# Optimization experiments

Hardware: AMD Instinct MI355X
Metric: run time of the kernel (lower is better)

Reference implementation:

```python
import jax, jax.numpy as jnp
import numpy as np

M_MARGIN = 0.25
GAMMA = 256.0
NEG_INF = jnp.float32(-1e30)


def setup_inputs() -> dict:
    key = jax.random.key(0)
    k1, k2 = jax.random.split(key)
    feature = jax.random.normal(k1, (8192, 128), dtype=jnp.float32)
    label = jax.random.randint(k2, (8192,), 0, 64, dtype=jnp.int64)
    return {"feature": feature, "label": label}


def reference(feature, label):
    # F.normalize: L2-normalize rows (eps=1e-12)
    norm = jnp.maximum(jnp.linalg.norm(feature, axis=1, keepdims=True), 1e-12)
    f = feature / norm
    sim = f @ f.T  # [N, N]
    N = sim.shape[0]

    same = label[:, None] == label[None, :]
    triu = jnp.triu(jnp.ones((N, N), dtype=bool), k=1)
    pos_mask = same & triu
    neg_mask = (~same) & triu

    sim_d = jax.lax.stop_gradient(sim)  # .detach() in original
    ap = jnp.maximum(-sim_d + 1.0 + M_MARGIN, 0.0)
    an = jnp.maximum(sim_d + M_MARGIN, 0.0)
    delta_p = 1.0 - M_MARGIN
    delta_n = M_MARGIN

    logit_p = -ap * (sim - delta_p) * GAMMA
    logit_n = an * (sim - delta_n) * GAMMA

    # boolean-gather + logsumexp == masked logsumexp (fixed shapes, jit-friendly)
    lse_p = jax.nn.logsumexp(jnp.where(pos_mask, logit_p, NEG_INF))
    lse_n = jax.nn.logsumexp(jnp.where(neg_mask, logit_n, NEG_INF))

    return jax.nn.softplus(lse_n + lse_p)
```

## Files before the change

### kernel.cpp

```cpp
#include <hip/hip_runtime.h>
#include <hip/hip_bf16.h>
#include <math.h>

#define NROW 8192
#define DIM  128
#define BT   128
#define NT   (NROW / BT)
#define NBLK ((NT * (NT + 1)) / 2)
#define NT4  (NBLK * 8)
#define NRED   32
#define PERRED (NT4 / NRED)

typedef __bf16 bf16x8 __attribute__((ext_vector_type(8)));
typedef float  f32x4  __attribute__((ext_vector_type(4)));

#define G2     369.3299304675746f
#define QPOS   (0.9375f * G2)
#define QNEG   (-0.0625f * G2)
#define NEGBIG (-3.0e38f)
#define MSENT  (-4000.0f)

__global__ __launch_bounds__(256)
void prep_kernel(const float* __restrict__ f, __hip_bfloat16* __restrict__ fhi) {
    int row  = blockIdx.x * 4 + (threadIdx.x >> 6);
    int lane = threadIdx.x & 63;
    float2 v = ((const float2*)(f + (size_t)row * DIM))[lane];
    float ss = v.x * v.x + v.y * v.y;
    #pragma unroll
    for (int off = 32; off; off >>= 1) ss += __shfl_xor(ss, off, 64);
    float inv = 1.0f / fmaxf(sqrtf(ss), 1e-12f);
    __hip_bfloat162 hv;
    hv.x = __float2bfloat16(v.x * inv);
    hv.y = __float2bfloat16(v.y * inv);
    ((__hip_bfloat162*)(fhi + (size_t)row * DIM))[lane] = hv;
}

__global__ __launch_bounds__(512, 4)
void sim_kernel(const __hip_bfloat16* __restrict__ fhi,
                const int* __restrict__ lab,
                float4* __restrict__ blockRes) {
    const int tid  = threadIdx.x;
    const int w    = tid >> 6;
    const int lane = tid & 63;
    const int lrow = lane & 15;
    const int lk   = lane >> 4;

    int bid = blockIdx.x;
    int tr = (int)((129.0f - sqrtf(16641.0f - 8.0f * (float)bid)) * 0.5f);
    while (tr > 0 && bid < tr * NT - (tr * (tr - 1)) / 2) --tr;
    while (bid >= (tr + 1) * NT - ((tr + 1) * tr) / 2) ++tr;
    const int tc = tr + (bid - (tr * NT - (tr * (tr - 1)) / 2));

    const int rowBase = tr * BT;
    const int colBase = tc * BT;
    const bool edge = (tr == tc);

    __shared__ __align__(16) char smem[64 * 1024];
    __shared__ int labA[BT];
    __shared__ int labB[BT];
    char* As = smem;
    char* Bs = smem + 32 * 1024;

    if (tid < BT)            labA[tid] = lab[rowBase + tid];
    else if (tid < 2 * BT)   labB[tid - BT] = lab[colBase + (tid - BT)];

    const int rsub4 = lane >> 4;
    const int col16 = (lane & 15) << 4;

    #pragma unroll
    for (int t = 0; t < 8; ++t) {
        int seg = w * 8 + t;
        int arr = seg >> 5;
        int s32 = seg & 31;
        int row = s32 * 4 + rsub4;
        const char* g = (const char*)fhi
            + (size_t)((arr ? colBase : rowBase) + row) * 256
            + (col16 ^ ((row & 7) << 4));
        char* ldsb = (arr ? Bs : As) + s32 * 1024;
        __builtin_amdgcn_global_load_lds(
            (const __attribute__((address_space(1))) void*)g,
            (__attribute__((address_space(3))) void*)ldsb, 16, 0, 0);
    }

    f32x4 acc[4][2];
    #pragma unroll
    for (int mi = 0; mi < 4; ++mi)
        #pragma unroll
        for (int ni = 0; ni < 2; ++ni) acc[mi][ni] = (f32x4){0.f, 0.f, 0.f, 0.f};

    const int mrow0 = (w >> 2) * 64;
    const int ncol0 = (w & 3) * 32;

    __syncthreads();

    #pragma unroll
    for (int q = 0; q < 4; ++q) {
        const int kb = q * 64 + lk * 16;
        bf16x8 bfr[2];
        #pragma unroll
        for (int ni = 0; ni < 2; ++ni) {
            int rb = ncol0 + ni * 16 + lrow;
            bfr[ni] = *(const bf16x8*)(Bs + rb * 256 + (kb ^ ((rb & 7) << 4)));
        }
        #pragma unroll
        for (int mi = 0; mi < 4; ++mi) {
            int ra = mrow0 + mi * 16 + lrow;
            bf16x8 afr = *(const bf16x8*)(As + ra * 256 + (kb ^ ((ra & 7) << 4)));
            #pragma unroll
            for (int ni = 0; ni < 2; ++ni)
                acc[mi][ni] = __builtin_amdgcn_mfma_f32_16x16x32_bf16(
                    afr, bfr[ni], acc[mi][ni], 0, 0, 0);
        }
    }

    int lbv[2];
    #pragma unroll
    for (int ni = 0; ni < 2; ++ni) lbv[ni] = labB[ncol0 + ni * 16 + lrow];
    int4 laR[4];
    #pragma unroll
    for (int mi = 0; mi < 4; ++mi)
        laR[mi] = *(const int4*)&labA[mrow0 + mi * 16 + lk * 4];

    float minp = 1e30f;
    float mabs = -1.0f;

#define PASS_A(EDGEF)                                                          \
    _Pragma("unroll")                                                          \
    for (int mi = 0; mi < 4; ++mi) {                                           \
        const int la[4] = {laR[mi].x, laR[mi].y, laR[mi].z, laR[mi].w};        \
        _Pragma("unroll")                                                      \
        for (int ni = 0; ni < 2; ++ni) {                                       \
            _Pragma("unroll")                                                  \
            for (int r = 0; r < 4; ++r) {                                      \
                float s = acc[mi][ni][r];                                      \
                bool pos = (la[r] == lbv[ni]);                                 \
                float t = fmaxf(s, -0.25f);                                    \
                bool valid = true;                                             \
                if (EDGEF) {                                                   \
                    int il = mrow0 + mi * 16 + lk * 4 + r;                     \
                    int jl = ncol0 + ni * 16 + lrow;                           \
                    valid = (jl > il);                                         \
                    pos = pos && valid;                                        \
                }                                                              \
                float u = pos ? s : t;                                         \
                minp = fminf(minp, pos ? s : 1e30f);                           \
                bool nm = EDGEF ? (valid && !pos) : !pos;                      \
                mabs = fmaxf(mabs, nm ? fabsf(t) : -1.0f);                     \
                acc[mi][ni][r] = u;                                            \
            }                                                                  \
        }                                                                      \
    }
    if (edge) { PASS_A(true) } else { PASS_A(false) }
#undef PASS_A

    #pragma unroll
    for (int off = 32; off; off >>= 1) {
        minp = fminf(minp, __shfl_xor(minp, off, 64));
        mabs = fmaxf(mabs, __shfl_xor(mabs, off, 64));
    }
    const float Mp = (minp < 2.0f)
        ? fmaf(G2, minp * minp, fmaf(-2.0f * G2, minp, QPOS)) : MSENT;
    const float Mn = (mabs >= 0.0f) ? fmaf(G2, mabs * mabs, QNEG) : MSENT;
    const float qph = QPOS - Mp;
    const float qnh = QNEG - Mn;
    float sp = 0.f, sn = 0.f;

#define PASS_B(EDGEF)                                                          \
    _Pragma("unroll")                                                          \
    for (int mi = 0; mi < 4; ++mi) {                                           \
        const int la[4] = {laR[mi].x, laR[mi].y, laR[mi].z, laR[mi].w};        \
        _Pragma("unroll")                                                      \
        for (int ni = 0; ni < 2; ++ni) {                                       \
            _Pragma("unroll")                                                  \
            for (int r = 0; r < 4; ++r) {                                      \
                float u = acc[mi][ni][r];                                      \
                bool pos = (la[r] == lbv[ni]);                                 \
                float P  = pos ? (-2.0f * G2) : 0.0f;                          \
                float Qh = pos ? qph : qnh;                                    \
                float e = __builtin_amdgcn_exp2f(                              \
                              fmaf(G2, u * u, fmaf(P, u, Qh)));                \
                if (EDGEF) {                                                   \
                    int il = mrow0 + mi * 16 + lk * 4 + r;                     \
                    int jl = ncol0 + ni * 16 + lrow;                           \
                    e = (jl > il) ? e : 0.f;                                   \
                }                                                              \
                float ep = pos ? e : 0.f;                                      \
                sp += ep;                                                      \
                sn += (e - ep);                                                \
            }                                                                  \
        }                                                                      \
    }
    if (edge) { PASS_B(true) } else { PASS_B(false) }
#undef PASS_B

    #pragma unroll
    for (int off = 32; off; off >>= 1) {
        sp += __shfl_xor(sp, off, 64);
        sn += __shfl_xor(sn, off, 64);
    }
    if (lane == 0) blockRes[bid * 8 + w] = make_float4(Mp, sp, Mn, sn);
}

__device__ __forceinline__ void merge2(float& m, float& s, float mo, float so) {
    float M = fmaxf(m, mo);
    s = s * __builtin_amdgcn_exp2f(m - M) + so * __builtin_amdgcn_exp2f(mo - M);
    m = M;
}

__global__ __launch_bounds__(256)
void reduce_kernel(const float4* __restrict__ in, float4* __restrict__ partial) {
    __shared__ float red[4][4];
    const int tid  = threadIdx.x;
    const int base = blockIdx.x * PERRED;
    float mp = NEGBIG, sp = 0.f, mn = NEGBIG, sn = 0.f;
    for (int i = tid; i < PERRED; i += 256) {
        float4 v = in[base + i];
        merge2(mp, sp, v.x, v.y);
        merge2(mn, sn, v.z, v.w);
    }
    #pragma unroll
    for (int off = 32; off; off >>= 1) {
        float mo = __shfl_xor(mp, off, 64), so = __shfl_xor(sp, off, 64);
        merge2(mp, sp, mo, so);
        float mo2 = __shfl_xor(mn, off, 64), so2 = __shfl_xor(sn, off, 64);
        merge2(mn, sn, mo2, so2);
    }
    const int wv = tid >> 6;
    if ((tid & 63) == 0) {
        red[wv][0] = mp; red[wv][1] = sp; red[wv][2] = mn; red[wv][3] = sn;
    }
    __syncthreads();
    if (tid == 0) {
        mp = red[0][0]; sp = red[0][1]; mn = red[0][2]; sn = red[0][3];
        #pragma unroll
        for (int q = 1; q < 4; ++q) {
            merge2(mp, sp, red[q][0], red[q][1]);
            merge2(mn, sn, red[q][2], red[q][3]);
        }
        partial[blockIdx.x] = make_float4(mp, sp, mn, sn);
    }
}

__global__ __launch_bounds__(64)
void finalize_kernel(const float4* __restrict__ partial, float* __restrict__ out) {
    const int lane = threadIdx.x;
    float mp = NEGBIG, sp = 0.f, mn = NEGBIG, sn = 0.f;
    if (lane < NRED) {
        float4 v = partial[lane];
        mp = v.x; sp = v.y; mn = v.z; sn = v.w;
    }
    #pragma unroll
    for (int off = 32; off; off >>= 1) {
        float mo = __shfl_xor(mp, off, 64), so = __shfl_xor(sp, off, 64);
        merge2(mp, sp, mo, so);
        float mo2 = __shfl_xor(mn, off, 64), so2 = __shfl_xor(sn, off, 64);
        merge2(mn, sn, mo2, so2);
    }
    if (lane == 0) {
        const double LN2 = 0.6931471805599453;
        double lse_p = ((double)mp + log2((double)sp)) * LN2;
        double lse_n = ((double)mn + log2((double)sn)) * LN2;
        double xx = lse_p + lse_n;
        double r = (xx > 30.0) ? xx : log1p(exp(xx));
        out[0] = (float)r;
    }
}

extern "C" void kernel_launch(void* const* d_in, const int* in_sizes, int n_in,
                              void* d_out, int out_size, void* d_ws, size_t ws_size,
                              hipStream_t stream) {
    const float* f   = (const float*)d_in[0];
    const int*   lab = (const int*)d_in[1];
    float*  out      = (float*)d_out;

    __hip_bfloat16* fhi = (__hip_bfloat16*)d_ws;
    float4* blockRes = (float4*)((char*)d_ws + 4u * 1024 * 1024);
    float4* partial  = (float4*)((char*)d_ws + 8u * 1024 * 1024);

    prep_kernel<<<NROW / 4, 256, 0, stream>>>(f, fhi);
    sim_kernel<<<NBLK, 512, 0, stream>>>(fhi, lab, blockRes);
    reduce_kernel<<<NRED, 256, 0, stream>>>(blockRes, partial);
    finalize_kernel<<<1, 64, 0, stream>>>(partial, out);
}
```

Measured before the change: 45.43 us.

## Give each wave its own 64x64 triangle tile and merge reduction kernels

Replaces the 128x128 block tile shared by 8 waves with independent per-wave 64x64 upper-triangle tiles. Each wave stages its own A and B slices through private LDS in two K-halves, so no block-level barrier is needed and the diagonal waste is finer-grained. Labels are read straight from global memory. The two-stage reduce plus finalize kernels become a single 1024-thread final kernel that does a global max and then a rescaled sum. The trade-off is less B-operand reuse across waves and more global traffic per output, plus one fewer kernel launch.

```diff
diff --git a/kernel.cpp b/kernel.cpp
--- a/kernel.cpp
+++ b/kernel.cpp
@@ -4,12 +4,10 @@
 
 #define NROW 8192
 #define DIM  128
-#define BT   128
-#define NT   (NROW / BT)
-#define NBLK ((NT * (NT + 1)) / 2)
-#define NT4  (NBLK * 8)
-#define NRED   32
-#define PERRED (NT4 / NRED)
+#define WT   64
+#define NTW  (NROW / WT)
+#define NWTILE ((NTW * (NTW + 1)) / 2)
+#define NBLK  (NWTILE / 4)
 
 typedef __bf16 bf16x8 __attribute__((ext_vector_type(8)));
 typedef float  f32x4  __attribute__((ext_vector_type(4)));
@@ -35,91 +33,99 @@
     ((__hip_bfloat162*)(fhi + (size_t)row * DIM))[lane] = hv;
 }
 
-__global__ __launch_bounds__(512, 4)
+__global__ __launch_bounds__(256, 2)
 void sim_kernel(const __hip_bfloat16* __restrict__ fhi,
                 const int* __restrict__ lab,
-                float4* __restrict__ blockRes) {
+                float4* __restrict__ waveRes) {
     const int tid  = threadIdx.x;
     const int w    = tid >> 6;
     const int lane = tid & 63;
     const int lrow = lane & 15;
     const int lk   = lane >> 4;
 
-    int bid = blockIdx.x;
-    int tr = (int)((129.0f - sqrtf(16641.0f - 8.0f * (float)bid)) * 0.5f);
-    while (tr > 0 && bid < tr * NT - (tr * (tr - 1)) / 2) --tr;
-    while (bid >= (tr + 1) * NT - ((tr + 1) * tr) / 2) ++tr;
-    const int tc = tr + (bid - (tr * NT - (tr * (tr - 1)) / 2));
-
-    const int rowBase = tr * BT;
-    const int colBase = tc * BT;
+    const int g = blockIdx.x * 4 + w;
+    int tr = (int)((257.0f - sqrtf(fmaxf(66049.0f - 8.0f * (float)g, 0.f))) * 0.5f);
+    if (tr > 127) tr = 127;
+    if (tr < 0) tr = 0;
+    while (tr > 0 && g < tr * NTW - (tr * (tr - 1)) / 2) --tr;
+    while (g >= (tr + 1) * NTW - ((tr + 1) * tr) / 2) ++tr;
+    const int tc = tr + (g - (tr * NTW - (tr * (tr - 1)) / 2));
+
+    const int rowBase = tr * WT;
+    const int colBase = tc * WT;
     const bool edge = (tr == tc);
 
-    __shared__ __align__(16) char smem[64 * 1024];
-    __shared__ int labA[BT];
-    __shared__ int labB[BT];
-    char* As = smem;
-    char* Bs = smem + 32 * 1024;
-
-    if (tid < BT)            labA[tid] = lab[rowBase + tid];
-    else if (tid < 2 * BT)   labB[tid - BT] = lab[colBase + (tid - BT)];
-
-    const int rsub4 = lane >> 4;
-    const int col16 = (lane & 15) << 4;
-
-    #pragma unroll
-    for (int t = 0; t < 8; ++t) {
-        int seg = w * 8 + t;
-        int arr = seg >> 5;
-        int s32 = seg & 31;
-        int row = s32 * 4 + rsub4;
-        const char* g = (const char*)fhi
-            + (size_t)((arr ? colBase : rowBase) + row) * 256
-            + (col16 ^ ((row & 7) << 4));
-        char* ldsb = (arr ? Bs : As) + s32 * 1024;
-        __builtin_amdgcn_global_load_lds(
-            (const __attribute__((address_space(1))) void*)g,
-            (__attribute__((address_space(3))) void*)ldsb, 16, 0, 0);
-    }
-
-    f32x4 acc[4][2];
+    __shared__ __align__(16) char smem[4 * 16384];
+    char* Abase = smem + w * 16384;
+    char* Bbase = Abase + 8192;
+
+    const int r8  = lane >> 3;
+    const int kbs = ((lane & 7) << 4) ^ (r8 << 4);
+
+    auto STAGE = [&](int c) {
+        #pragma unroll
+        for (int s = 0; s < 8; ++s) {
+            int row = s * 8 + r8;
+            const char* ga = (const char*)fhi + (size_t)(rowBase + row) * 256
+                           + c * 128 + kbs;
+            __builtin_amdgcn_global_load_lds(
+                (const __attribute__((address_space(1))) void*)ga,
+                (__attribute__((address_space(3))) void*)(Abase + s * 1024), 16, 0, 0);
+        }
+        #pragma unroll
+        for (int s = 0; s < 8; ++s) {
+            int row = s * 8 + r8;
+            const char* gb = (const char*)fhi + (size_t)(colBase + row) * 256
+                           + c * 128 + kbs;
+            __builtin_amdgcn_global_load_lds(
+                (const __attribute__((address_space(1))) void*)gb,
+                (__attribute__((address_space(3))) void*)(Bbase + s * 1024), 16, 0, 0);
+        }
+    };
+
+    f32x4 acc[4][4];
     #pragma unroll
     for (int mi = 0; mi < 4; ++mi)
         #pragma unroll
-        for (int ni = 0; ni < 2; ++ni) acc[mi][ni] = (f32x4){0.f, 0.f, 0.f, 0.f};
-
-    const int mrow0 = (w >> 2) * 64;
-    const int ncol0 = (w & 3) * 32;
-
-    __syncthreads();
-
-    #pragma unroll
-    for (int q = 0; q < 4; ++q) {
-        const int kb = q * 64 + lk * 16;
-        bf16x8 bfr[2];
-        #pragma unroll
-        for (int ni = 0; ni < 2; ++ni) {
-            int rb = ncol0 + ni * 16 + lrow;
-            bfr[ni] = *(const bf16x8*)(Bs + rb * 256 + (kb ^ ((rb & 7) << 4)));
+        for (int ni = 0; ni < 4; ++ni) acc[mi][ni] = (f32x4){0.f, 0.f, 0.f, 0.f};
+
+    auto COMPUTE = [&]() {
+        #pragma unroll
+        for (int q = 0; q < 2; ++q) {
+            const int kb = q * 64 + lk * 16;
+            bf16x8 bfr[4];
+            #pragma unroll
+            for (int ni = 0; ni < 4; ++ni) {
+                int rb = ni * 16 + lrow;
+                bfr[ni] = *(const bf16x8*)(Bbase + rb * 128 + (kb ^ ((rb & 7) << 4)));
+            }
+            #pragma unroll
+            for (int mi = 0; mi < 4; ++mi) {
+                int ra = mi * 16 + lrow;
+                bf16x8 afr = *(const bf16x8*)(Abase + ra * 128 + (kb ^ ((ra & 7) << 4)));
+                #pragma unroll
+                for (int ni = 0; ni < 4; ++ni)
+                    acc[mi][ni] = __builtin_amdgcn_mfma_f32_16x16x32_bf16(
+                        afr, bfr[ni], acc[mi][ni], 0, 0, 0);
+            }
         }
-        #pragma unroll
-        for (int mi = 0; mi < 4; ++mi) {
-            int ra = mrow0 + mi * 16 + lrow;
-            bf16x8 afr = *(const bf16x8*)(As + ra * 256 + (kb ^ ((ra & 7) << 4)));
-            #pragma unroll
-            for (int ni = 0; ni < 2; ++ni)
-                acc[mi][ni] = __builtin_amdgcn_mfma_f32_16x16x32_bf16(
-                    afr, bfr[ni], acc[mi][ni], 0, 0, 0);
-        }
-    }
-
-    int lbv[2];
-    #pragma unroll
-    for (int ni = 0; ni < 2; ++ni) lbv[ni] = labB[ncol0 + ni * 16 + lrow];
+    };
+
+    STAGE(0);
+    int lbv[4];
+    #pragma unroll
+    for (int ni = 0; ni < 4; ++ni) lbv[ni] = lab[colBase + ni * 16 + lrow];
     int4 laR[4];
     #pragma unroll
     for (int mi = 0; mi < 4; ++mi)
-        laR[mi] = *(const int4*)&labA[mrow0 + mi * 16 + lk * 4];
+        laR[mi] = *(const int4*)&lab[rowBase + mi * 16 + lk * 4];
+
+    asm volatile("s_waitcnt vmcnt(0)" ::: "memory");
+    COMPUTE();
+    asm volatile("s_waitcnt lgkmcnt(0)" ::: "memory");
+    STAGE(1);
+    asm volatile("s_waitcnt vmcnt(0)" ::: "memory");
+    COMPUTE();
 
     float minp = 1e30f;
     float mabs = -1.0f;
@@ -129,7 +135,7 @@
     for (int mi = 0; mi < 4; ++mi) {                                           \
         const int la[4] = {laR[mi].x, laR[mi].y, laR[mi].z, laR[mi].w};        \
         _Pragma("unroll")                                                      \
-        for (int ni = 0; ni < 2; ++ni) {                                       \
+        for (int ni = 0; ni < 4; ++ni) {                                       \
             _Pragma("unroll")                                                  \
             for (int r = 0; r < 4; ++r) {                                      \
                 float s = acc[mi][ni][r];                                      \
@@ -137,8 +143,8 @@
                 float t = fmaxf(s, -0.25f);                                    \
                 bool valid = true;                                             \
                 if (EDGEF) {                                                   \
-                    int il = mrow0 + mi * 16 + lk * 4 + r;                     \
-                    int jl = ncol0 + ni * 16 + lrow;                           \
+                    int il = mi * 16 + lk * 4 + r;                             \
+                    int jl = ni * 16 + lrow;                                   \
                     valid = (jl > il);                                         \
                     pos = pos && valid;                                        \
                 }                                                              \
@@ -170,7 +176,7 @@
     for (int mi = 0; mi < 4; ++mi) {                                           \
         const int la[4] = {laR[mi].x, laR[mi].y, laR[mi].z, laR[mi].w};        \
         _Pragma("unroll")                                                      \
-        for (int ni = 0; ni < 2; ++ni) {                                       \
+        for (int ni = 0; ni < 4; ++ni) {                                       \
             _Pragma("unroll")                                                  \
             for (int r = 0; r < 4; ++r) {                                      \
                 float u = acc[mi][ni][r];                                      \
@@ -180,8 +186,8 @@
                 float e = __builtin_amdgcn_exp2f(                              \
                               fmaf(G2, u * u, fmaf(P, u, Qh)));                \
                 if (EDGEF) {                                                   \
-                    int il = mrow0 + mi * 16 + lk * 4 + r;                     \
-                    int jl = ncol0 + ni * 16 + lrow;                           \
+                    int il = mi * 16 + lk * 4 + r;                             \
+                    int jl = ni * 16 + lrow;                                   \
                     e = (jl > il) ? e : 0.f;                                   \
                 }                                                              \
                 float ep = pos ? e : 0.f;                                      \
@@ -198,68 +204,59 @@
         sp += __shfl_xor(sp, off, 64);
         sn += __shfl_xor(sn, off, 64);
     }
-    if (lane == 0) blockRes[bid * 8 + w] = make_float4(Mp, sp, Mn, sn);
-}
-
-__device__ __forceinline__ void merge2(float& m, float& s, float mo, float so) {
-    float M = fmaxf(m, mo);
-    s = s * __builtin_amdgcn_exp2f(m - M) + so * __builtin_amdgcn_exp2f(mo - M);
-    m = M;
-}
-
-__global__ __launch_bounds__(256)
-void reduce_kernel(const float4* __restrict__ in, float4* __restrict__ partial) {
-    __shared__ float red[4][4];
+    if (lane == 0) waveRes[g] = make_float4(Mp, sp, Mn, sn);
+}
+
+__global__ __launch_bounds__(1024)
+void final_kernel(const float4* __restrict__ waveRes, float* __restrict__ out) {
+    __shared__ float red[16][4];
     const int tid  = threadIdx.x;
-    const int base = blockIdx.x * PERRED;
-    float mp = NEGBIG, sp = 0.f, mn = NEGBIG, sn = 0.f;
-    for (int i = tid; i < PERRED; i += 256) {
-        float4 v = in[base + i];
-        merge2(mp, sp, v.x, v.y);
-        merge2(mn, sn, v.z, v.w);
-    }
-    #pragma unroll
-    for (int off = 32; off; off >>= 1) {
-        float mo = __shfl_xor(mp, off, 64), so = __shfl_xor(sp, off, 64);
-        merge2(mp, sp, mo, so);
-        float mo2 = __shfl_xor(mn, off, 64), so2 = __shfl_xor(sn, off, 64);
-        merge2(mn, sn, mo2, so2);
-    }
-    const int wv = tid >> 6;
-    if ((tid & 63) == 0) {
-        red[wv][0] = mp; red[wv][1] = sp; red[wv][2] = mn; red[wv][3] = sn;
-    }
+    const int wv   = tid >> 6;
+    const int lane = tid & 63;
+
+    float4 e[9];
+    int ne = 0;
+    for (int i = tid; i < NWTILE; i += 1024) e[ne++] = waveRes[i];
+
+    float mp = NEGBIG, mn = NEGBIG;
+    for (int k = 0; k < ne; ++k) {
+        mp = fmaxf(mp, e[k].x);
+        mn = fmaxf(mn, e[k].z);
+    }
+    #pragma unroll
+    for (int off = 32; off; off >>= 1) {
+        mp = fmaxf(mp, __shfl_xor(mp, off, 64));
+        mn = fmaxf(mn, __shfl_xor(mn, off, 64));
+    }
+    if (lane == 0) { red[wv][0] = mp; red[wv][1] = mn; }
+    __syncthreads();
+    float MP = red[0][0], MN = red[0][1];
+    #pragma unroll
+    for (int q = 1; q < 16; ++q) {
+        MP = fmaxf(MP, red[q][0]);
+        MN = fmaxf(MN, red[q][1]);
+    }
+
+    float sp = 0.f, sn = 0.f;
+    for (int k = 0; k < ne; ++k) {
+        sp = fmaf(e[k].y, __builtin_amdgcn_exp2f(e[k].x - MP), sp);
+        sn = fmaf(e[k].w, __builtin_amdgcn_exp2f(e[k].z - MN), sn);
+    }
+    #pragma unroll
+    for (int off = 32; off; off >>= 1) {
+        sp += __shfl_xor(sp, off, 64);
+        sn += __shfl_xor(sn, off, 64);
+    }
+    __syncthreads();
+    if (lane == 0) { red[wv][2] = sp; red[wv][3] = sn; }
     __syncthreads();
     if (tid == 0) {
-        mp = red[0][0]; sp = red[0][1]; mn = red[0][2]; sn = red[0][3];
-        #pragma unroll
-        for (int q = 1; q < 4; ++q) {
-            merge2(mp, sp, red[q][0], red[q][1]);
-            merge2(mn, sn, red[q][2], red[q][3]);
-        }
-        partial[blockIdx.x] = make_float4(mp, sp, mn, sn);
-    }
-}
-
-__global__ __launch_bounds__(64)
-void finalize_kernel(const float4* __restrict__ partial, float* __restrict__ out) {
-    const int lane = threadIdx.x;
-    float mp = NEGBIG, sp = 0.f, mn = NEGBIG, sn = 0.f;
-    if (lane < NRED) {
-        float4 v = partial[lane];
-        mp = v.x; sp = v.y; mn = v.z; sn = v.w;
-    }
-    #pragma unroll
-    for (int off = 32; off; off >>= 1) {
-        float mo = __shfl_xor(mp, off, 64), so = __shfl_xor(sp, off, 64);
-        merge2(mp, sp, mo, so);
-        float mo2 = __shfl_xor(mn, off, 64), so2 = __shfl_xor(sn, off, 64);
-        merge2(mn, sn, mo2, so2);
-    }
-    if (lane == 0) {
+        float Sp = 0.f, Sn = 0.f;
+        #pragma unroll
+        for (int q = 0; q < 16; ++q) { Sp += red[q][2]; Sn += red[q][3]; }
         const double LN2 = 0.6931471805599453;
-        double lse_p = ((double)mp + log2((double)sp)) * LN2;
-        double lse_n = ((double)mn + log2((double)sn)) * LN2;
+        double lse_p = ((double)MP + log2((double)Sp)) * LN2;
+        double lse_n = ((double)MN + log2((double)Sn)) * LN2;
         double xx = lse_p + lse_n;
         double r = (xx > 30.0) ? xx : log1p(exp(xx));
         out[0] = (float)r;
@@ -274,11 +271,9 @@
     float*  out      = (float*)d_out;
 
     __hip_bfloat16* fhi = (__hip_bfloat16*)d_ws;
-    float4* blockRes = (float4*)((char*)d_ws + 4u * 1024 * 1024);
-    float4* partial  = (float4*)((char*)d_ws + 8u * 1024 * 1024);
+    float4* waveRes = (float4*)((char*)d_ws + 4u * 1024 * 1024);
 
     prep_kernel<<<NROW / 4, 256, 0, stream>>>(f, fhi);
-    sim_kernel<<<NBLK, 512, 0, stream>>>(fhi, lab, blockRes);
-    reduce_kernel<<<NRED, 256, 0, stream>>>(blockRes, partial);
-    finalize_kernel<<<1, 64, 0, stream>>>(partial, out);
-}
+    sim_kernel<<<NBLK, 256, 0, stream>>>(fhi, lab, waveRes);
+    final_kernel<<<1, 1024, 0, stream>>>(waveRes, out);
+}
```

Result: slower. 54.29 us (+19.5%).
